# Kernel tuning notes

Measured on AMD Instinct MI355X. Metric: run time of the kernel, lower is better.

## Reference

```python
import math
import jax, jax.numpy as jnp
import numpy as np

NUM_ANGLE = 8
NUM_RADIAL = 3
RADIAL_MIN = 0.08
RADIAL_MAX = 0.9
EPS = 1e-6


def _hann(n):
    # torch.hann_window(n, periodic=False)
    return 0.5 * (1.0 - jnp.cos(2.0 * jnp.pi * jnp.arange(n, dtype=jnp.float32) / (n - 1)))


def _to_luma(img):
    # img: [B, 3, H, W] -> [B, H, W]
    return 0.2989 * img[:, 0] + 0.587 * img[:, 1] + 0.114 * img[:, 2]


def _log_magnitude(img):
    x = _to_luma(img).astype(jnp.float32)  # [B, H, W]
    H, W = x.shape[-2], x.shape[-1]
    win = _hann(H)[:, None] * _hann(W)[None, :]  # [H, W]
    x = x * win
    spec = jnp.fft.fftshift(jnp.fft.fft2(x, axes=(-2, -1)), axes=(-2, -1))
    return jnp.log1p(jnp.abs(spec))  # [B, H, W]


def _polar_masks(H, W):
    y = jnp.linspace(-1.0, 1.0, H, dtype=jnp.float32)
    x = jnp.linspace(-1.0, 1.0, W, dtype=jnp.float32)
    yy, xx = jnp.meshgrid(y, x, indexing='ij')
    radius = jnp.sqrt(xx * xx + yy * yy)
    radius = radius / jnp.maximum(radius.max(), EPS)
    angle = jnp.remainder(jnp.arctan2(yy, xx), math.pi)

    r_edges = jnp.linspace(RADIAL_MIN, RADIAL_MAX, NUM_RADIAL + 1, dtype=jnp.float32)
    a_edges = jnp.linspace(0.0, math.pi, NUM_ANGLE + 1, dtype=jnp.float32)

    r0 = r_edges[:-1][:, None, None]
    r1 = r_edges[1:][:, None, None]
    rmask = (radius[None] >= r0) & (radius[None] < r1)           # [R, H, W]
    rmask = rmask.at[-1].set((radius >= r_edges[-2]) & (radius <= r_edges[-1]))

    t0 = a_edges[:-1][:, None, None]
    t1 = a_edges[1:][:, None, None]
    amask = (angle[None] >= t0) & (angle[None] < t1)             # [A, H, W]
    amask = amask.at[-1].set((angle >= a_edges[-2]) & (angle <= a_edges[-1]))

    return (rmask[:, None] & amask[None, :]).astype(jnp.float32)  # [R, A, H, W]


def _sector_energies(img):
    mag = _log_magnitude(img)                          # [B, H, W]
    masks = _polar_masks(mag.shape[-2], mag.shape[-1])  # [R, A, H, W]
    mask_sum = jnp.maximum(masks.sum(axis=(-2, -1)), EPS)        # [R, A]
    masked_sum = jnp.einsum('bhw,rahw->bra', mag, masks)         # [B, R, A]
    energies = masked_sum / mask_sum[None]
    energies = energies / jnp.maximum(energies.sum(axis=-1, keepdims=True), EPS)
    return energies


def setup_inputs() -> dict:
    key = jax.random.key(0)
    k1, k2 = jax.random.split(key)
    B, C, H, W = 16, 3, 512, 512
    prediction = jax.random.uniform(k1, (B, C, H, W), dtype=jnp.float32)
    target = jax.random.uniform(k2, (B, C, H, W), dtype=jnp.float32)
    radial_weights = jnp.array([0.5, 1.0, 1.2], dtype=jnp.float32).reshape(1, NUM_RADIAL, 1)
    return {"prediction": prediction, "target": target, "radial_weights": radial_weights}


def reference(prediction, target, radial_weights):
    pred_e = _sector_energies(prediction)   # [B, R, A]
    tgt_e = _sector_energies(target)
    diff = pred_e - tgt_e
    dist = jnp.sqrt(diff * diff + EPS)      # charbonnier
    return (dist * radial_weights).mean()
```

## Files before the change

### kernel.cpp

```cpp
#include <hip/hip_runtime.h>
#include <math.h>

#define PI_F 3.14159265358979323846f
#define TWO_PI_F 6.28318530717958647692f
#define RSQ2 0.70710678118654752440f

#define WAVE_SYNC() __asm__ volatile("s_waitcnt lgkmcnt(0)" ::: "memory")
#define LADDR(a) ((a) + ((a) >> 3))

__device__ __forceinline__ float2 cadd(float2 a, float2 b){ return make_float2(a.x+b.x, a.y+b.y); }
__device__ __forceinline__ float2 csub(float2 a, float2 b){ return make_float2(a.x-b.x, a.y-b.y); }
__device__ __forceinline__ float2 cmul(float2 a, float2 b){ return make_float2(a.x*b.x - a.y*b.y, a.x*b.y + a.y*b.x); }
__device__ __forceinline__ float2 cw1(float2 a){ return make_float2(RSQ2*(a.x+a.y), RSQ2*(a.y-a.x)); }
__device__ __forceinline__ float2 cw2(float2 a){ return make_float2(a.y, -a.x); }
__device__ __forceinline__ float2 cw3(float2 a){ return make_float2(RSQ2*(a.y-a.x), -RSQ2*(a.x+a.y)); }

__device__ __forceinline__ void dft8(float2* v){
    float2 a0=cadd(v[0],v[4]), a1=cadd(v[1],v[5]), a2=cadd(v[2],v[6]), a3=cadd(v[3],v[7]);
    float2 b0=csub(v[0],v[4]);
    float2 b1=cw1(csub(v[1],v[5]));
    float2 b2=cw2(csub(v[2],v[6]));
    float2 b3=cw3(csub(v[3],v[7]));
    float2 c0=cadd(a0,a2), c2=csub(a0,a2), c1=cadd(a1,a3), c3=cw2(csub(a1,a3));
    float2 d0=cadd(b0,b2), d2=csub(b0,b2), d1=cadd(b1,b3), d3=cw2(csub(b1,b3));
    v[0]=cadd(c0,c1); v[1]=csub(c0,c1);
    v[2]=cadd(c2,c3); v[3]=csub(c2,c3);
    v[4]=cadd(d0,d1); v[5]=csub(d0,d1);
    v[6]=cadd(d2,d3); v[7]=csub(d2,d3);
}

__device__ __forceinline__ void stage_store(float2* wl, const float2* v, float2 w1,
                                            int base, int step){
    constexpr int br[8] = {0,4,2,6,1,5,3,7};
    wl[LADDR(base)] = v[0];
    float2 p = w1;
    #pragma unroll
    for (int c = 1; c < 8; ++c) {
        wl[LADDR(base + step*c)] = cmul(v[br[c]], p);
        p = cmul(p, w1);
    }
}

__device__ __forceinline__ void stage_load(const float2* wl, float2* v, int j){
    #pragma unroll
    for (int i = 0; i < 8; ++i) v[i] = wl[LADDR(j + 64*i)];
}

__device__ __forceinline__ int sector_id(int hm, int wm) {
    const float step = 2.0f / 511.0f;
    float y = -1.0f + step * (float)hm;
    float x = -1.0f + step * (float)wm;
    float radius = sqrtf(x * x + y * y);
    float r = radius / sqrtf(2.0f);
    float a = atan2f(y, x);
    a = fmodf(a, PI_F);
    if (a < 0.0f) a += PI_F;

    const float rstep = (0.9f - 0.08f) / 3.0f;
    const float re0 = 0.08f;
    const float re1 = 0.08f + rstep;
    const float re2 = 0.08f + 2.0f * rstep;
    const float re3 = 0.9f;
    int rb;
    if      (r >= re0 && r < re1)  rb = 0;
    else if (r >= re1 && r < re2)  rb = 1;
    else if (r >= re2 && r <= re3) rb = 2;
    else return -1;

    const float astep = PI_F / 8.0f;
    int ab = 7;
    #pragma unroll
    for (int i = 0; i < 7; ++i) {
        float t0 = astep * (float)i;
        float t1 = astep * (float)(i + 1);
        if (a >= t0 && a < t1) { ab = i; break; }
    }
    return rb * 8 + ab;
}

__device__ __forceinline__ float hannf(int i) {
    return 0.5f * (1.0f - __cosf(TWO_PI_F * (float)i / 511.0f));
}

__global__ void zero_kernel(float* p, int n) {
    int i = blockIdx.x * 256 + threadIdx.x;
    if (i < n) p[i] = 0.0f;
}

__global__ __launch_bounds__(256) void rowfft_kernel(const float* __restrict__ pred,
                                                     const float* __restrict__ tgt,
                                                     float4* __restrict__ out4,
                                                     unsigned char* __restrict__ mapT,
                                                     float* __restrict__ counts) {
    __shared__ float2 lds[4 * 576];
    __shared__ float cbins[24];
    int blk = blockIdx.x;
    int img = blk >> 6;
    int pb  = blk & 63;
    int t = threadIdx.x;
    int wv = t >> 6, j = t & 63;
    int hp = pb * 4 + wv;
    int h0 = 2 * hp;
    float2* wl = lds + wv * 576;

    if (t < 24) cbins[t] = 0.0f;
    __syncthreads();
    if (t < 128) {
        int idx = blk * 128 + t;
        int wm = idx >> 9, hm = idx & 511;
        int s = sector_id(hm, wm);
        mapT[idx] = (unsigned char)(s < 0 ? 255 : s);
        if (s >= 0) atomicAdd(&cbins[s], 1.0f);
    }

    const float* base = (img < 16) ? (pred + (size_t)img * 786432)
                                   : (tgt  + (size_t)(img - 16) * 786432);
    float wh0 = hannf(h0), wh1 = hannf(h0 + 1);
    float2 v[8];
    #pragma unroll
    for (int i = 0; i < 8; ++i) {
        int w = j + 64 * i;
        float ww = hannf(w);
        size_t off0 = (size_t)h0 * 512 + w;
        size_t off1 = off0 + 512;
        float l0 = 0.2989f*base[off0] + 0.587f*base[off0+262144] + 0.114f*base[off0+524288];
        float l1 = 0.2989f*base[off1] + 0.587f*base[off1+262144] + 0.114f*base[off1+524288];
        v[i] = make_float2(l0 * (wh0 * ww), l1 * (wh1 * ww));
    }
    float sn, cs;
    dft8(v);
    __sincosf(-TWO_PI_F * (float)j / 512.0f, &sn, &cs);
    stage_store(wl, v, make_float2(cs, sn), 8 * j, 1);
    WAVE_SYNC();
    stage_load(wl, v, j);
    WAVE_SYNC();
    dft8(v);
    __sincosf(-TWO_PI_F * (float)((j >> 3) << 3) / 512.0f, &sn, &cs);
    stage_store(wl, v, make_float2(cs, sn), (j & 7) + 64 * (j >> 3), 8);
    WAVE_SYNC();
    stage_load(wl, v, j);
    dft8(v);
    constexpr int br[8] = {0,4,2,6,1,5,3,7};
    size_t kbase = (size_t)img * 257;
    int partner = (64 - j) & 63;
    #pragma unroll
    for (int c = 0; c < 4; ++c) {
        float2 zk = v[br[c]];
        float mx = __shfl(v[br[7 - c]].x, partner, 64);
        float my = __shfl(v[br[7 - c]].y, partner, 64);
        float2 zs = v[br[(8 - c) & 7]];
        float2 zm = make_float2(j == 0 ? zs.x : mx, j == 0 ? zs.y : my);
        int k = j + 64 * c;
        float4 o = make_float4(0.5f*(zk.x+zm.x), 0.5f*(zk.y-zm.y),
                               0.5f*(zk.y+zm.y), 0.5f*(zm.x-zk.x));
        out4[(kbase + k) * 256 + hp] = o;
    }
    if (j == 0) {
        float2 z = v[br[4]];
        out4[(kbase + 256) * 256 + hp] = make_float4(z.x, 0.0f, z.y, 0.0f);
    }
    __syncthreads();
    if (t < 24) {
        float c = cbins[t];
        if (c != 0.0f) atomicAdd(&counts[t], c);
    }
}

__global__ __launch_bounds__(256) void colfft_kernel(const float2* __restrict__ buf,
                                                     const unsigned char* __restrict__ mapT,
                                                     float* __restrict__ acc) {
    __shared__ float2 lds[4 * 576];
    __shared__ float bins[4 * 200];
    int t = threadIdx.x;
    int wv = t >> 6, j = t & 63;
    int gid = blockIdx.x * 4 + wv;
    int img = gid / 257;
    int w = gid - img * 257;
    float2* wl = lds + wv * 576;
    float* wb = bins + wv * 200;
    #pragma unroll
    for (int i = 0; i < 4; ++i) {
        int ii = j + 64 * i;
        if (ii < 200) wb[ii] = 0.0f;
    }
    const float2* col = buf + (size_t)gid * 512;
    float2 v[8];
    #pragma unroll
    for (int i = 0; i < 8; ++i) v[i] = col[j + 64 * i];
    float sn, cs;
    dft8(v);
    __sincosf(-TWO_PI_F * (float)j / 512.0f, &sn, &cs);
    stage_store(wl, v, make_float2(cs, sn), 8 * j, 1);
    WAVE_SYNC();
    stage_load(wl, v, j);
    WAVE_SYNC();
    dft8(v);
    __sincosf(-TWO_PI_F * (float)((j >> 3) << 3) / 512.0f, &sn, &cs);
    stage_store(wl, v, make_float2(cs, sn), (j & 7) + 64 * (j >> 3), 8);
    WAVE_SYNC();
    stage_load(wl, v, j);
    dft8(v);
    constexpr int br[8] = {0,4,2,6,1,5,3,7};
    const unsigned char* mw  = mapT + (size_t)((w + 256) & 511) * 512;
    const unsigned char* mw2 = mapT + (size_t)((256 - w) & 511) * 512;
    bool mir = (w >= 1 && w <= 255);
    int rep = (j & 7) * 25;
    #pragma unroll
    for (int c = 0; c < 8; ++c) {
        float2 z = v[br[c]];
        float mag = log1pf(sqrtf(z.x * z.x + z.y * z.y));
        int hm = j + 64 * ((c + 4) & 7);
        int s1 = mw[hm];
        if (s1 < 24) atomicAdd(&wb[rep + s1], mag);
        if (mir) {
            int hm2 = (256 - (j + 64 * c)) & 511;
            int s2 = mw2[hm2];
            if (s2 < 24) atomicAdd(&wb[rep + s2], mag);
        }
    }
    WAVE_SYNC();
    if (j < 24) {
        float sum = 0.0f;
        #pragma unroll
        for (int r = 0; r < 8; ++r) sum += wb[r * 25 + j];
        atomicAdd(&acc[img * 24 + j], sum);
    }
}

__global__ __launch_bounds__(384) void final_kernel(const float* __restrict__ acc,
                                                    const float* __restrict__ counts,
                                                    const float* __restrict__ rw,
                                                    float* __restrict__ out) {
    __shared__ float ep[384], et[384], red[384];
    int t = threadIdx.x;
    int b = t / 24;
    int s = t % 24;
    int r = s >> 3;
    float cnt = fmaxf(counts[s], 1e-6f);
    ep[t] = acc[b * 24 + s] / cnt;
    et[t] = acc[(16 + b) * 24 + s] / cnt;
    __syncthreads();
    int gbase = b * 24 + r * 8;
    float sp = 0.0f, st = 0.0f;
    #pragma unroll
    for (int a = 0; a < 8; ++a) { sp += ep[gbase + a]; st += et[gbase + a]; }
    float pe = ep[t] / fmaxf(sp, 1e-6f);
    float te = et[t] / fmaxf(st, 1e-6f);
    float d = pe - te;
    float dist = sqrtf(d * d + 1e-6f);
    red[t] = dist * rw[r];
    __syncthreads();
    if (t < 128) red[t] += red[t + 128] + red[t + 256];
    __syncthreads();
    if (t < 64) {
        float v = red[t] + red[t + 64];
        #pragma unroll
        for (int o = 32; o > 0; o >>= 1) v += __shfl_down(v, o, 64);
        if (t == 0) out[0] = v / 384.0f;
    }
}

extern "C" void kernel_launch(void* const* d_in, const int* in_sizes, int n_in,
                              void* d_out, int out_size, void* d_ws, size_t ws_size,
                              hipStream_t stream) {
    const float* pred = (const float*)d_in[0];
    const float* tgt  = (const float*)d_in[1];
    const float* rw   = (const float*)d_in[2];

    char* ws = (char*)d_ws;
    float* acc    = (float*)ws;
    float* counts = acc + 32 * 24;
    unsigned char* mapT = (unsigned char*)(ws + 4096);
    float2* buf   = (float2*)(ws + 4096 + 262144);

    zero_kernel<<<4, 256, 0, stream>>>(acc, 32 * 24 + 24);
    rowfft_kernel<<<32 * 64, 256, 0, stream>>>(pred, tgt, (float4*)buf, mapT, counts);
    colfft_kernel<<<2056, 256, 0, stream>>>(buf, mapT, acc);
    final_kernel<<<1, 384, 0, stream>>>(acc, counts, rw, (float*)d_out);
}
```

Before: 205.1 us.

## Stage row-FFT output through LDS for coalesced stores, widen bins, drop waitcnts

The row FFT kernel now transposes its four-wave output through shared memory so that consecutive threads write consecutive float4s in global memory, replacing the strided per-wave stores. The sector-count bins become per-wave, which removes an early block barrier. The column kernel raises the number of replicated LDS bins from 8 to 16 to reduce atomic contention. The explicit s_waitcnt lgkmcnt(0) syncs are replaced by compiler-only fences, which relies on the compiler inserting the needed waits within a wave and could be a correctness risk.

```diff
diff --git a/kernel.cpp b/kernel.cpp
--- a/kernel.cpp
+++ b/kernel.cpp
@@ -5,7 +5,7 @@
 #define TWO_PI_F 6.28318530717958647692f
 #define RSQ2 0.70710678118654752440f
 
-#define WAVE_SYNC() __asm__ volatile("s_waitcnt lgkmcnt(0)" ::: "memory")
+#define CFENCE() __asm__ volatile("" ::: "memory")
 #define LADDR(a) ((a) + ((a) >> 3))
 
 __device__ __forceinline__ float2 cadd(float2 a, float2 b){ return make_float2(a.x+b.x, a.y+b.y); }
@@ -93,7 +93,7 @@
                                                      unsigned char* __restrict__ mapT,
                                                      float* __restrict__ counts) {
     __shared__ float2 lds[4 * 576];
-    __shared__ float cbins[24];
+    __shared__ float cbins[4 * 24];
     int blk = blockIdx.x;
     int img = blk >> 6;
     int pb  = blk & 63;
@@ -102,15 +102,15 @@
     int hp = pb * 4 + wv;
     int h0 = 2 * hp;
     float2* wl = lds + wv * 576;
-
-    if (t < 24) cbins[t] = 0.0f;
-    __syncthreads();
-    if (t < 128) {
-        int idx = blk * 128 + t;
+    float* wc = cbins + wv * 24;
+
+    if (j < 24) wc[j] = 0.0f;
+    if (j < 32) {
+        int idx = (blk * 4 + wv) * 32 + j;
         int wm = idx >> 9, hm = idx & 511;
         int s = sector_id(hm, wm);
         mapT[idx] = (unsigned char)(s < 0 ? 255 : s);
-        if (s >= 0) atomicAdd(&cbins[s], 1.0f);
+        if (s >= 0) atomicAdd(&wc[s], 1.0f);
     }
 
     const float* base = (img < 16) ? (pred + (size_t)img * 786432)
@@ -131,18 +131,19 @@
     dft8(v);
     __sincosf(-TWO_PI_F * (float)j / 512.0f, &sn, &cs);
     stage_store(wl, v, make_float2(cs, sn), 8 * j, 1);
-    WAVE_SYNC();
-    stage_load(wl, v, j);
-    WAVE_SYNC();
+    CFENCE();
+    stage_load(wl, v, j);
+    CFENCE();
     dft8(v);
     __sincosf(-TWO_PI_F * (float)((j >> 3) << 3) / 512.0f, &sn, &cs);
     stage_store(wl, v, make_float2(cs, sn), (j & 7) + 64 * (j >> 3), 8);
-    WAVE_SYNC();
-    stage_load(wl, v, j);
+    CFENCE();
+    stage_load(wl, v, j);
+    CFENCE();
     dft8(v);
     constexpr int br[8] = {0,4,2,6,1,5,3,7};
-    size_t kbase = (size_t)img * 257;
     int partner = (64 - j) & 63;
+    float4 o[4];
     #pragma unroll
     for (int c = 0; c < 4; ++c) {
         float2 zk = v[br[c]];
@@ -150,39 +151,50 @@
         float my = __shfl(v[br[7 - c]].y, partner, 64);
         float2 zs = v[br[(8 - c) & 7]];
         float2 zm = make_float2(j == 0 ? zs.x : mx, j == 0 ? zs.y : my);
-        int k = j + 64 * c;
-        float4 o = make_float4(0.5f*(zk.x+zm.x), 0.5f*(zk.y-zm.y),
-                               0.5f*(zk.y+zm.y), 0.5f*(zm.x-zk.x));
-        out4[(kbase + k) * 256 + hp] = o;
-    }
+        o[c] = make_float4(0.5f*(zk.x+zm.x), 0.5f*(zk.y-zm.y),
+                           0.5f*(zk.y+zm.y), 0.5f*(zm.x-zk.x));
+    }
+    float4 oext;
     if (j == 0) {
         float2 z = v[br[4]];
-        out4[(kbase + 256) * 256 + hp] = make_float4(z.x, 0.0f, z.y, 0.0f);
-    }
-    __syncthreads();
-    if (t < 24) {
-        float c = cbins[t];
-        if (c != 0.0f) atomicAdd(&counts[t], c);
-    }
-}
-
+        oext = make_float4(z.x, 0.0f, z.y, 0.0f);
+    }
+    CFENCE();
+    if (j < 24) {
+        float c = wc[j];
+        if (c != 0.0f) atomicAdd(&counts[j], c);
+    }
+    __syncthreads();
+    float4* trans = (float4*)lds;
+    #pragma unroll
+    for (int c = 0; c < 4; ++c) trans[(j + 64 * c) * 4 + wv] = o[c];
+    if (j == 0) trans[256 * 4 + wv] = oext;
+    __syncthreads();
+    size_t kb = (size_t)img * 257;
+    int hpb = pb * 4;
+    #pragma unroll
+    for (int m = 0; m < 4; ++m) {
+        int idx = t + 256 * m;
+        int k = idx >> 2, hpL = idx & 3;
+        out4[(kb + k) * 256 + hpb + hpL] = trans[idx];
+    }
+    if (t < 4) out4[(kb + 256) * 256 + hpb + t] = trans[1024 + t];
+}
+
+#define NREP 16
 __global__ __launch_bounds__(256) void colfft_kernel(const float2* __restrict__ buf,
                                                      const unsigned char* __restrict__ mapT,
                                                      float* __restrict__ acc) {
     __shared__ float2 lds[4 * 576];
-    __shared__ float bins[4 * 200];
+    __shared__ float bins[4 * NREP * 25];
     int t = threadIdx.x;
     int wv = t >> 6, j = t & 63;
     int gid = blockIdx.x * 4 + wv;
     int img = gid / 257;
     int w = gid - img * 257;
     float2* wl = lds + wv * 576;
-    float* wb = bins + wv * 200;
-    #pragma unroll
-    for (int i = 0; i < 4; ++i) {
-        int ii = j + 64 * i;
-        if (ii < 200) wb[ii] = 0.0f;
-    }
+    float* wb = bins + wv * NREP * 25;
+    for (int i = j; i < NREP * 25; i += 64) wb[i] = 0.0f;
     const float2* col = buf + (size_t)gid * 512;
     float2 v[8];
     #pragma unroll
@@ -191,20 +203,21 @@
     dft8(v);
     __sincosf(-TWO_PI_F * (float)j / 512.0f, &sn, &cs);
     stage_store(wl, v, make_float2(cs, sn), 8 * j, 1);
-    WAVE_SYNC();
-    stage_load(wl, v, j);
-    WAVE_SYNC();
+    CFENCE();
+    stage_load(wl, v, j);
+    CFENCE();
     dft8(v);
     __sincosf(-TWO_PI_F * (float)((j >> 3) << 3) / 512.0f, &sn, &cs);
     stage_store(wl, v, make_float2(cs, sn), (j & 7) + 64 * (j >> 3), 8);
-    WAVE_SYNC();
-    stage_load(wl, v, j);
+    CFENCE();
+    stage_load(wl, v, j);
+    CFENCE();
     dft8(v);
     constexpr int br[8] = {0,4,2,6,1,5,3,7};
     const unsigned char* mw  = mapT + (size_t)((w + 256) & 511) * 512;
     const unsigned char* mw2 = mapT + (size_t)((256 - w) & 511) * 512;
     bool mir = (w >= 1 && w <= 255);
-    int rep = (j & 7) * 25;
+    int rep = (j & (NREP - 1)) * 25;
     #pragma unroll
     for (int c = 0; c < 8; ++c) {
         float2 z = v[br[c]];
@@ -218,11 +231,11 @@
             if (s2 < 24) atomicAdd(&wb[rep + s2], mag);
         }
     }
-    WAVE_SYNC();
+    CFENCE();
     if (j < 24) {
         float sum = 0.0f;
         #pragma unroll
-        for (int r = 0; r < 8; ++r) sum += wb[r * 25 + j];
+        for (int r = 0; r < NREP; ++r) sum += wb[r * 25 + j];
         atomicAdd(&acc[img * 24 + j], sum);
     }
 }
```

New measurement: 242.3 us. +18.1%, slower.
